# Kernel optimization log

Measured on AMD Instinct MI355X. Metric: run time of the kernel, lower is better.

## Reference

```python
import jax, jax.numpy as jnp
import numpy as np

B, S, E, H = 2, 2048, 512, 8
D = E // H
BETA = 0.5
SCALE = float(np.sqrt(D))


def setup_inputs() -> dict:
    key = jax.random.key(0)
    ks = jax.random.split(key, 22)
    inp = {}
    for i, n in enumerate(["qx", "qy", "kx", "ky", "vx", "vy"]):
        inp[n] = jax.random.normal(ks[i], (B, S, E), jnp.float32)
    wnames = ["Wqx", "Wqy", "Wkx", "Wky", "Wvx", "Wvy", "Wox", "Woy"]
    for i, n in enumerate(wnames):
        inp[n] = jax.random.normal(ks[6 + i], (E, E), jnp.float32) * 0.02
        inp["b" + n[1:]] = jnp.zeros((E,), jnp.float32)
    return inp


def _split_heads(x):
    # [B, S, E] -> [B, H, S, D]
    return x.reshape(B, S, H, D).transpose(0, 2, 1, 3)


def _merge_heads(x):
    # [B, H, S, D] -> [B, S, E]
    return x.transpose(0, 2, 1, 3).reshape(B, S, E)


def reference(qx, qy, kx, ky, vx, vy,
              Wqx, bqx, Wqy, bqy, Wkx, bkx, Wky, bky,
              Wvx, bvx, Wvy, bvy, Wox, box, Woy, boy):
    lin = lambda x, W, b: x @ W.T + b  # torch nn.Linear convention
    qxh = _split_heads(lin(qx, Wqx, bqx))
    qyh = _split_heads(lin(qy, Wqy, bqy))
    kxh = _split_heads(lin(kx, Wkx, bkx))
    kyh = _split_heads(lin(ky, Wky, bky))
    vxh = _split_heads(lin(vx, Wvx, bvx))
    vyh = _split_heads(lin(vy, Wvy, bvy))

    # polar decomposition of the bichannel: radius, angle
    aq = jnp.arctan2(qyh, qxh)  # [B,H,S,D]
    ak = jnp.arctan2(kyh, kxh)
    # mean_d cos(aq - ak) == (cos_q @ cos_k^T + sin_q @ sin_k^T) / D
    # (avoids the [B,H,Sq,Sk,D] angle_diff tensor; same math)
    phase = (jnp.einsum('bhqd,bhkd->bhqk', jnp.cos(aq), jnp.cos(ak))
             + jnp.einsum('bhqd,bhkd->bhqk', jnp.sin(aq), jnp.sin(ak))) / D

    rq = jnp.sqrt(qxh * qxh + qyh * qyh)
    rk = jnp.sqrt(kxh * kxh + kyh * kyh)
    mag = jnp.einsum('bhqd,bhkd->bhqk', rq, rk) / SCALE

    scores = BETA * phase + (1.0 - BETA) * mag  # [B,H,Sq,Sk]
    attn = jax.nn.softmax(scores, axis=-1)      # dropout is identity in eval

    ax = _merge_heads(jnp.einsum('bhqk,bhkd->bhqd', attn, vxh))
    ay = _merge_heads(jnp.einsum('bhqk,bhkd->bhqd', attn, vyh))
    return lin(ax, Wox, box), lin(ay, Woy, boy)
```

## Files before the change

kernel.cpp:

```cpp
#include <hip/hip_runtime.h>
#include <hip/hip_bf16.h>


#define N_ROWS 4096
#define EDIM 512
#define SEQ 2048
#define NHEAD 8
#define HDIM 64
#define CDIM 192
#define DV 128

#define PHASE_A 0.08838834764831845f
#define MAG_B   0.25f
#define SM_SHIFT 8.0f

typedef _Float16 half8 __attribute__((ext_vector_type(8)));
typedef float f32x4 __attribute__((ext_vector_type(4)));

__device__ inline void gload16(const void* g, void* l) {
    __builtin_amdgcn_global_load_lds(
        (const __attribute__((address_space(1))) unsigned int*)g,
        (__attribute__((address_space(3))) unsigned int*)l, 16, 0, 0);
}

#define KSW(r) (((((r) & 3) | (((r) >> 1) & 4))) << 4)

struct Cvt8 { const float* s[8]; _Float16* d[8]; };

__global__ __launch_bounds__(256) void cvt_fp16(Cvt8 j, int n8) {
    const float* s = j.s[blockIdx.y];
    _Float16* d = j.d[blockIdx.y];
    union U { _Float16 h[8]; uint4 u; };
    for (int i = blockIdx.x * 256 + threadIdx.x; i < n8; i += gridDim.x * 256) {
        const float4 f0 = ((const float4*)s)[2 * i];
        const float4 f1 = ((const float4*)s)[2 * i + 1];
        U u;
        u.h[0] = (_Float16)f0.x; u.h[1] = (_Float16)f0.y;
        u.h[2] = (_Float16)f0.z; u.h[3] = (_Float16)f0.w;
        u.h[4] = (_Float16)f1.x; u.h[5] = (_Float16)f1.y;
        u.h[6] = (_Float16)f1.z; u.h[7] = (_Float16)f1.w;
        ((uint4*)d)[i] = u.u;
    }
}

struct PairArgs {
    const void* x0;     const void* x1;
    const _Float16* w0; const _Float16* w1;
    const float* b0;    const float* b1;
    void* dst0;         void* dst1;
};

template <int FUSED>
__global__ __launch_bounds__(256, 3) void gemm16(PairArgs A0, PairArgs A1, PairArgs A2)
{
    __shared__ _Float16 smem[2][12288];

    const int tid = threadIdx.x;
    const int w = tid >> 6, l = tid & 63;
    const int g = l >> 4, ql = l & 15;
    const int wr = w >> 1, wc = w & 1;

    const int dd = blockIdx.x;
    const int xcd = dd & 7;
    const int sb = dd >> 3;
    int z_, mt, nb;
    if (FUSED) {
        const int zm = xcd * 12 + (sb >> 3);
        nb = sb & 7;
        z_ = zm >> 5;
        mt = zm & 31;
    } else {
        z_ = 0;
        mt = xcd * 4 + (sb >> 3);
        nb = sb & 7;
    }
    const PairArgs& A = FUSED ? (z_ == 0 ? A0 : (z_ == 1 ? A1 : A2)) : A0;
    const int z = z_;
    const int m0 = mt * 128;
    const int n0 = nb * 64;

    size_t srcA[2];
    #pragma unroll
    for (int i = 0; i < 2; ++i) {
        const int s = i * 256 + tid;
        const int row = s >> 2, c = s & 3;
        const int cs = c ^ ((row >> 1) & 3);
        srcA[i] = (size_t)(m0 + row) * EDIM + cs * 8;
    }
    const int rowB = tid >> 2;
    const int csB = (tid & 3) ^ ((rowB >> 1) & 3);
    const size_t srcB = (size_t)(n0 + rowB) * EDIM + csB * 8;

    const float* x0f = (const float*)A.x0;
    const float* x1f = (const float*)A.x1;
    const _Float16* x0h = (const _Float16*)A.x0;
    const _Float16* x1h = (const _Float16*)A.x1;

    float4 xr[2][2][2];

    #define LOADX(k0)                                                         \
        do { _Pragma("unroll")                                                \
          for (int i = 0; i < 2; ++i) {                                       \
              const float* p0 = x0f + srcA[i] + (k0);                         \
              const float* p1 = x1f + srcA[i] + (k0);                         \
              xr[0][i][0] = *(const float4*)p0;                               \
              xr[0][i][1] = *(const float4*)(p0 + 4);                         \
              xr[1][i][0] = *(const float4*)p1;                               \
              xr[1][i][1] = *(const float4*)(p1 + 4);                         \
          } } while (0)
    #define WRITEX(buf)                                                       \
        do { _Pragma("unroll")                                                \
          for (int arr = 0; arr < 2; ++arr) {                                 \
              _Pragma("unroll")                                               \
              for (int i = 0; i < 2; ++i) {                                   \
                  union { _Float16 h[8]; uint4 u; } t;                        \
                  _Pragma("unroll")                                           \
                  for (int jj = 0; jj < 4; ++jj) {                            \
                      t.h[jj]     = (_Float16)xr[arr][i][0][jj];              \
                      t.h[4 + jj] = (_Float16)xr[arr][i][1][jj];              \
                  }                                                           \
                  *(uint4*)&smem[buf][arr * 4096 + (i * 256 + tid) * 8] = t.u;\
              } } } while (0)
    #define STAGEX_LDS(buf, k0)                                               \
        do { _Pragma("unroll")                                                \
          for (int i = 0; i < 2; ++i) {                                       \
              gload16(x0h + srcA[i] + (k0),                                   \
                      &smem[buf][(i * 256 + w * 64) * 8]);                    \
              gload16(x1h + srcA[i] + (k0),                                   \
                      &smem[buf][4096 + (i * 256 + w * 64) * 8]);             \
          } } while (0)
    #define STAGEW(buf, k0)                                                   \
        do { gload16(A.w0 + srcB + (k0), &smem[buf][8192 + w * 512]);         \
             gload16(A.w1 + srcB + (k0), &smem[buf][10240 + w * 512]); } while (0)

    f32x4 acc0[4][2], acc1[4][2];
    #pragma unroll
    for (int f = 0; f < 4; ++f)
        #pragma unroll
        for (int e = 0; e < 2; ++e) {
            acc0[f][e] = (f32x4){0.f, 0.f, 0.f, 0.f};
            acc1[f][e] = (f32x4){0.f, 0.f, 0.f, 0.f};
        }

    auto COMPUTE = [&](int buf) {
        half8 af0[4], af1[4], bf0[2], bf1[2];
        #pragma unroll
        for (int f = 0; f < 4; ++f) {
            const int arow = wr * 64 + f * 16 + ql;
            const int ho = arow * 32 + (g ^ ((arow >> 1) & 3)) * 8;
            af0[f] = *(const half8*)&smem[buf][ho];
            af1[f] = *(const half8*)&smem[buf][4096 + ho];
        }
        #pragma unroll
        for (int e = 0; e < 2; ++e) {
            const int brow = wc * 32 + e * 16 + ql;
            const int ho = brow * 32 + (g ^ ((brow >> 1) & 3)) * 8;
            bf0[e] = *(const half8*)&smem[buf][8192 + ho];
            bf1[e] = *(const half8*)&smem[buf][10240 + ho];
        }
        #pragma unroll
        for (int f = 0; f < 4; ++f)
            #pragma unroll
            for (int e = 0; e < 2; ++e) {
                acc0[f][e] = __builtin_amdgcn_mfma_f32_16x16x32_f16(
                    af0[f], bf0[e], acc0[f][e], 0, 0, 0);
                acc1[f][e] = __builtin_amdgcn_mfma_f32_16x16x32_f16(
                    af1[f], bf1[e], acc1[f][e], 0, 0, 0);
            }
    };

    if (FUSED) {
        LOADX(0);
        WRITEX(0);
    } else {
        STAGEX_LDS(0, 0);
    }
    STAGEW(0, 0);

    for (int k0 = 0; k0 < EDIM; k0 += 32) {
        const int cur = (k0 >> 5) & 1, nxt = cur ^ 1;
        __syncthreads();
        const bool more = (k0 + 32) < EDIM;
        if (more) {
            if (FUSED) {
                LOADX(k0 + 32);
            } else {
                STAGEX_LDS(nxt, k0 + 32);
            }
            STAGEW(nxt, k0 + 32);
        }
        COMPUTE(cur);
        if (more && FUSED) {
            WRITEX(nxt);
        }
    }
    #undef LOADX
    #undef WRITEX
    #undef STAGEX_LDS
    #undef STAGEW

    #pragma unroll
    for (int f = 0; f < 4; ++f) {
        const int mb = m0 + wr * 64 + f * 16 + g * 4;
        #pragma unroll
        for (int e = 0; e < 2; ++e) {
            const int n = n0 + wc * 32 + e * 16 + ql;
            const float bias0 = A.b0[n];
            const float bias1 = A.b1[n];
            if (!FUSED) {
                float* o0 = (float*)A.dst0;
                float* o1 = (float*)A.dst1;
                #pragma unroll
                for (int r = 0; r < 4; ++r) {
                    const int m = mb + r;
                    o0[(size_t)m * EDIM + n] = acc0[f][e][r] + bias0;
                    o1[(size_t)m * EDIM + n] = acc1[f][e][r] + bias1;
                }
            } else {
                const int b = mb >> 11, s = mb & (SEQ - 1);
                const int h = nb;
                const int d = n & (HDIM - 1);
                const int bh = b * NHEAD + h;
                _Float16* dst = (_Float16*)A.dst0;
                if (z != 2) {
                    const size_t base = ((size_t)bh * SEQ + s) * CDIM + d;
                    #pragma unroll
                    for (int r = 0; r < 4; ++r) {
                        const float v0 = acc0[f][e][r] + bias0;
                        const float v1 = acc1[f][e][r] + bias1;
                        const float r2 = v0 * v0 + v1 * v1;
                        const float rm = sqrtf(r2);
                        float c, sn;
                        if (r2 > 0.f) { c = v0 / rm; sn = v1 / rm; }
                        else          { c = 1.f;     sn = 0.f; }
                        dst[base + (size_t)r * CDIM]       = (_Float16)(c  * PHASE_A);
                        dst[base + (size_t)r * CDIM + 64]  = (_Float16)(sn * PHASE_A);
                        dst[base + (size_t)r * CDIM + 128] = (_Float16)(rm * MAG_B);
                    }
                } else {
                    union Pk { _Float16 h[4]; uint2 u; } p0, p1;
                    #pragma unroll
                    for (int r = 0; r < 4; ++r) {
                        p0.h[r] = (_Float16)(acc0[f][e][r] + bias0);
                        p1.h[r] = (_Float16)(acc1[f][e][r] + bias1);
                    }
                    *(uint2*)&dst[((size_t)bh * DV + d) * SEQ + s]      = p0.u;
                    *(uint2*)&dst[((size_t)bh * DV + 64 + d) * SEQ + s] = p1.u;
                }
            }
        }
    }
}

__global__ __launch_bounds__(512, 2) void attn_mfma(
    const _Float16* __restrict__ Qg, const _Float16* __restrict__ Kg,
    const _Float16* __restrict__ Vg,
    _Float16* __restrict__ ax, _Float16* __restrict__ ay)
{
    __shared__ char smem[81920];

    const int tid = threadIdx.x;
    const int w  = tid >> 6;
    const int l  = tid & 63;
    const int g  = l >> 4;
    const int ql = l & 15;

    const int d  = blockIdx.x;
    const int xcd = d & 7;
    const int j   = d >> 3;
    const int bh  = xcd + 8 * (j >> 4);
    const int q0  = (j & 15) * 128;
    const int b  = bh >> 3, h = bh & 7;
    const int qrow = q0 + w * 16 + ql;

    half8 qf[6];
    {
        const char* qp = (const char*)(Qg + ((size_t)bh * SEQ + qrow) * CDIM);
        #pragma unroll
        for (int c = 0; c < 6; ++c) {
            uint4 u = *(const uint4*)(qp + c * 64 + g * 16);
            qf[c] = __builtin_bit_cast(half8, u);
        }
    }

    f32x4 o[8];
    #pragma unroll
    for (int vt = 0; vt < 8; ++vt) o[vt] = (f32x4){0.f, 0.f, 0.f, 0.f};
    float l_i = 0.f;

    const char* kgb = (const char*)(Kg + (size_t)bh * SEQ * CDIM);
    const char* vgb = (const char*)(Vg + (size_t)bh * DV * SEQ);

    int koff[3], vofs[2];
    #pragma unroll
    for (int i = 0; i < 3; ++i) {
        const int beta = (w * 3 + i) * 1024 + l * 16;
        const int r = beta / 384;
        const int cb = (beta - r * 384) ^ KSW(r);
        koff[i] = r * 384 + cb;
    }
    #pragma unroll
    for (int i = 0; i < 2; ++i) {
        const int beta = (w * 2 + i) * 1024 + l * 16;
        const int r = beta >> 7;
        const int cb = (beta & 127) ^ ((r & 7) << 4);
        vofs[i] = r * 4096 + cb;
    }

    const int rq = ((ql >> 2) << 3) + (ql & 3);
    const int kxor = ((ql & 3) | (((ql >> 2) & 1) << 2)) << 4;

    #define STAGE(kbase, vbase, kt0)                                          \
        do { _Pragma("unroll")                                                \
          for (int i = 0; i < 3; ++i)                                         \
              gload16(kgb + (size_t)(kt0) * 384 + koff[i],                    \
                      smem + (kbase) + (w * 3 + i) * 1024);                   \
          _Pragma("unroll")                                                   \
          for (int i = 0; i < 2; ++i)                                         \
              gload16(vgb + (size_t)(kt0) * 2 + vofs[i],                      \
                      smem + (vbase) + (w * 2 + i) * 1024); } while (0)

    auto COMPUTE = [&](const int kbase, const int vbase) {
        f32x4 st[4];
        __builtin_amdgcn_s_setprio(1);
        #pragma unroll
        for (int kt = 0; kt < 4; ++kt) {
            f32x4 acc = {0.f, 0.f, 0.f, 0.f};
            const int r_p = rq + (kt & 1) * 32 + ((kt >> 1) << 2);
            #pragma unroll
            for (int c = 0; c < 6; ++c) {
                uint4 u = *(const uint4*)(
                    smem + kbase + ((r_p * 384 + c * 64 + g * 16) ^ kxor));
                acc = __builtin_amdgcn_mfma_f32_16x16x32_f16(
                    __builtin_bit_cast(half8, u), qf[c], acc, 0, 0, 0);
            }
            st[kt] = acc;
        }
        __builtin_amdgcn_s_setprio(0);

        float rs = 0.f;
        #pragma unroll
        for (int kt = 0; kt < 4; ++kt)
            #pragma unroll
            for (int r = 0; r < 4; ++r) {
                const float p = __expf(st[kt][r] - SM_SHIFT);
                st[kt][r] = p; rs += p;
            }
        rs += __shfl_xor(rs, 16);
        rs += __shfl_xor(rs, 32);
        l_i += rs;

        half8 pf[2];
        #pragma unroll
        for (int ks = 0; ks < 2; ++ks) {
            union { _Float16 h[8]; half8 v; } u;
            u.h[0] = (_Float16)st[ks][0];     u.h[1] = (_Float16)st[ks][1];
            u.h[2] = (_Float16)st[ks][2];     u.h[3] = (_Float16)st[ks][3];
            u.h[4] = (_Float16)st[ks + 2][0]; u.h[5] = (_Float16)st[ks + 2][1];
            u.h[6] = (_Float16)st[ks + 2][2]; u.h[7] = (_Float16)st[ks + 2][3];
            pf[ks] = u.v;
        }

        __builtin_amdgcn_s_setprio(1);
        #pragma unroll
        for (int vt = 0; vt < 8; ++vt) {
            const int v = vt * 16 + ql;
            uint4 u0 = *(const uint4*)(
                smem + vbase + ((v * 128 + g * 16) ^ ((v & 7) << 4)));
            uint4 u1 = *(const uint4*)(
                smem + vbase + ((v * 128 + 64 + g * 16) ^ ((v & 7) << 4)));
            o[vt] = __builtin_amdgcn_mfma_f32_16x16x32_f16(
                pf[0], __builtin_bit_cast(half8, u0), o[vt], 0, 0, 0);
            o[vt] = __builtin_amdgcn_mfma_f32_16x16x32_f16(
                pf[1], __builtin_bit_cast(half8, u1), o[vt], 0, 0, 0);
        }
        __builtin_amdgcn_s_setprio(0);
    };

    STAGE(0, 49152, 0);
    for (int t = 0; t < 32; t += 2) {
        __syncthreads();
        STAGE(24576, 65536, (t + 1) * 64);
        COMPUTE(0, 49152);
        __syncthreads();
        if (t + 2 < 32) STAGE(0, 49152, (t + 2) * 64);
        COMPUTE(24576, 65536);
    }
    #undef STAGE

    const float invl = 1.f / l_i;
    const float fi0 = __shfl(invl, g * 4 + 0);
    const float fi1 = __shfl(invl, g * 4 + 1);
    const float fi2 = __shfl(invl, g * 4 + 2);
    const float fi3 = __shfl(invl, g * 4 + 3);
    #pragma unroll
    for (int vt = 0; vt < 8; ++vt) {
        const int v = vt * 16 + ql;
        _Float16* basep = (vt < 4) ? ax : ay;
        const int vv = v & 63;
        const float fi[4] = {fi0, fi1, fi2, fi3};
        #pragma unroll
        for (int r = 0; r < 4; ++r) {
            const int q = q0 + w * 16 + g * 4 + r;
            basep[((size_t)(b * SEQ + q)) * EDIM + h * HDIM + vv] =
                (_Float16)(o[vt][r] * fi[r]);
        }
    }
}

extern "C" void kernel_launch(void* const* d_in, const int* in_sizes, int n_in,
                              void* d_out, int out_size, void* d_ws, size_t ws_size,
                              hipStream_t stream)
{
    const float* act[6];
    for (int i = 0; i < 6; ++i) act[i] = (const float*)d_in[i];
    const float* W[8]; const float* Bv[8];
    for (int i = 0; i < 8; ++i) {
        W[i]  = (const float*)d_in[6 + 2 * i];
        Bv[i] = (const float*)d_in[7 + 2 * i];
    }

    float* outx = (float*)d_out;
    float* outy = outx + 2097152;

    _Float16* ws = (_Float16*)d_ws;
    _Float16* w16[8];
    for (int i = 0; i < 8; ++i) w16[i] = ws + (size_t)i * 262144;
    _Float16* Qt16 = ws + 2097152;
    _Float16* Kt16 = Qt16 + 6291456;
    _Float16* Vt16 = Kt16 + 6291456;
    _Float16* ax16 = Vt16 + 4194304;
    _Float16* ay16 = ax16 + 2097152;

    Cvt8 jw{};
    for (int i = 0; i < 8; ++i) { jw.s[i] = W[i]; jw.d[i] = w16[i]; }
    hipLaunchKernelGGL(cvt_fp16, dim3(128, 8), dim3(256), 0, stream, jw, 32768);

    PairArgs qa{act[0], act[1], w16[0], w16[1], Bv[0], Bv[1], Qt16, nullptr};
    PairArgs ka{act[2], act[3], w16[2], w16[3], Bv[2], Bv[3], Kt16, nullptr};
    PairArgs va{act[4], act[5], w16[4], w16[5], Bv[4], Bv[5], Vt16, nullptr};
    hipLaunchKernelGGL((gemm16<1>), dim3(768), dim3(256), 0, stream, qa, ka, va);

    hipLaunchKernelGGL(attn_mfma, dim3(256), dim3(512), 0, stream,
                       Qt16, Kt16, Vt16, ax16, ay16);

    PairArgs oa{ax16, ay16, w16[6], w16[7], Bv[6], Bv[7], outx, outy};
    hipLaunchKernelGGL((gemm16<0>), dim3(256), dim3(256), 0, stream, oa, oa, oa);
}
```

Measured before the change: 116.9 us.

## Process two query sub-tiles per wave in attention to reuse K/V fragments

The attention kernel now runs 4 waves of 256 threads instead of 8, and each wave handles 32 query rows as two 16-row halves. Each K and V fragment read from LDS feeds two MFMAs, which halves LDS read traffic per FLOP. Each thread now issues twice as many global-to-LDS staging loads. The cost is doubled accumulator and score registers per wave, half the waves per block, and launch bounds that allow only one block per CU, so there is less latency hiding.

```diff
diff --git a/kernel.cpp b/kernel.cpp
--- a/kernel.cpp
+++ b/kernel.cpp
@@ -252,7 +252,7 @@
     }
 }
 
-__global__ __launch_bounds__(512, 2) void attn_mfma(
+__global__ __launch_bounds__(256, 1) void attn_mfma(
     const _Float16* __restrict__ Qg, const _Float16* __restrict__ Kg,
     const _Float16* __restrict__ Vg,
     _Float16* __restrict__ ax, _Float16* __restrict__ ay)
@@ -271,37 +271,41 @@
     const int bh  = xcd + 8 * (j >> 4);
     const int q0  = (j & 15) * 128;
     const int b  = bh >> 3, h = bh & 7;
-    const int qrow = q0 + w * 16 + ql;
-
-    half8 qf[6];
-    {
+
+    half8 qf[2][6];
+    #pragma unroll
+    for (int hh = 0; hh < 2; ++hh) {
+        const int qrow = q0 + w * 32 + hh * 16 + ql;
         const char* qp = (const char*)(Qg + ((size_t)bh * SEQ + qrow) * CDIM);
         #pragma unroll
         for (int c = 0; c < 6; ++c) {
             uint4 u = *(const uint4*)(qp + c * 64 + g * 16);
-            qf[c] = __builtin_bit_cast(half8, u);
-        }
-    }
-
-    f32x4 o[8];
-    #pragma unroll
-    for (int vt = 0; vt < 8; ++vt) o[vt] = (f32x4){0.f, 0.f, 0.f, 0.f};
-    float l_i = 0.f;
+            qf[hh][c] = __builtin_bit_cast(half8, u);
+        }
+    }
+
+    f32x4 o0[8], o1[8];
+    #pragma unroll
+    for (int vt = 0; vt < 8; ++vt) {
+        o0[vt] = (f32x4){0.f, 0.f, 0.f, 0.f};
+        o1[vt] = (f32x4){0.f, 0.f, 0.f, 0.f};
+    }
+    float l_i0 = 0.f, l_i1 = 0.f;
 
     const char* kgb = (const char*)(Kg + (size_t)bh * SEQ * CDIM);
     const char* vgb = (const char*)(Vg + (size_t)bh * DV * SEQ);
 
-    int koff[3], vofs[2];
-    #pragma unroll
-    for (int i = 0; i < 3; ++i) {
-        const int beta = (w * 3 + i) * 1024 + l * 16;
+    int koff[6], vofs[4];
+    #pragma unroll
+    for (int i = 0; i < 6; ++i) {
+        const int beta = i * 4096 + w * 1024 + l * 16;
         const int r = beta / 384;
         const int cb = (beta - r * 384) ^ KSW(r);
         koff[i] = r * 384 + cb;
     }
     #pragma unroll
-    for (int i = 0; i < 2; ++i) {
-        const int beta = (w * 2 + i) * 1024 + l * 16;
+    for (int i = 0; i < 4; ++i) {
+        const int beta = i * 4096 + w * 1024 + l * 16;
         const int r = beta >> 7;
         const int cb = (beta & 127) ^ ((r & 7) << 4);
         vofs[i] = r * 4096 + cb;
@@ -312,67 +316,75 @@
 
     #define STAGE(kbase, vbase, kt0)                                          \
         do { _Pragma("unroll")                                                \
-          for (int i = 0; i < 3; ++i)                                         \
+          for (int i = 0; i < 6; ++i)                                         \
               gload16(kgb + (size_t)(kt0) * 384 + koff[i],                    \
-                      smem + (kbase) + (w * 3 + i) * 1024);                   \
+                      smem + (kbase) + i * 4096 + w * 1024);                  \
           _Pragma("unroll")                                                   \
-          for (int i = 0; i < 2; ++i)                                         \
+          for (int i = 0; i < 4; ++i)                                         \
               gload16(vgb + (size_t)(kt0) * 2 + vofs[i],                      \
-                      smem + (vbase) + (w * 2 + i) * 1024); } while (0)
+                      smem + (vbase) + i * 4096 + w * 1024); } while (0)
 
     auto COMPUTE = [&](const int kbase, const int vbase) {
-        f32x4 st[4];
+        f32x4 st0[4], st1[4];
         __builtin_amdgcn_s_setprio(1);
         #pragma unroll
         for (int kt = 0; kt < 4; ++kt) {
-            f32x4 acc = {0.f, 0.f, 0.f, 0.f};
+            f32x4 a0 = {0.f, 0.f, 0.f, 0.f};
+            f32x4 a1 = {0.f, 0.f, 0.f, 0.f};
             const int r_p = rq + (kt & 1) * 32 + ((kt >> 1) << 2);
             #pragma unroll
             for (int c = 0; c < 6; ++c) {
                 uint4 u = *(const uint4*)(
                     smem + kbase + ((r_p * 384 + c * 64 + g * 16) ^ kxor));
-                acc = __builtin_amdgcn_mfma_f32_16x16x32_f16(
-                    __builtin_bit_cast(half8, u), qf[c], acc, 0, 0, 0);
-            }
-            st[kt] = acc;
+                const half8 kf = __builtin_bit_cast(half8, u);
+                a0 = __builtin_amdgcn_mfma_f32_16x16x32_f16(kf, qf[0][c], a0, 0, 0, 0);
+                a1 = __builtin_amdgcn_mfma_f32_16x16x32_f16(kf, qf[1][c], a1, 0, 0, 0);
+            }
+            st0[kt] = a0; st1[kt] = a1;
         }
         __builtin_amdgcn_s_setprio(0);
 
-        float rs = 0.f;
+        float rs0 = 0.f, rs1 = 0.f;
         #pragma unroll
         for (int kt = 0; kt < 4; ++kt)
             #pragma unroll
             for (int r = 0; r < 4; ++r) {
-                const float p = __expf(st[kt][r] - SM_SHIFT);
-                st[kt][r] = p; rs += p;
-            }
-        rs += __shfl_xor(rs, 16);
-        rs += __shfl_xor(rs, 32);
-        l_i += rs;
-
-        half8 pf[2];
+                const float p0 = __expf(st0[kt][r] - SM_SHIFT);
+                const float p1 = __expf(st1[kt][r] - SM_SHIFT);
+                st0[kt][r] = p0; rs0 += p0;
+                st1[kt][r] = p1; rs1 += p1;
+            }
+        rs0 += __shfl_xor(rs0, 16); rs0 += __shfl_xor(rs0, 32); l_i0 += rs0;
+        rs1 += __shfl_xor(rs1, 16); rs1 += __shfl_xor(rs1, 32); l_i1 += rs1;
+
+        half8 pf0[2], pf1[2];
         #pragma unroll
         for (int ks = 0; ks < 2; ++ks) {
-            union { _Float16 h[8]; half8 v; } u;
-            u.h[0] = (_Float16)st[ks][0];     u.h[1] = (_Float16)st[ks][1];
-            u.h[2] = (_Float16)st[ks][2];     u.h[3] = (_Float16)st[ks][3];
-            u.h[4] = (_Float16)st[ks + 2][0]; u.h[5] = (_Float16)st[ks + 2][1];
-            u.h[6] = (_Float16)st[ks + 2][2]; u.h[7] = (_Float16)st[ks + 2][3];
-            pf[ks] = u.v;
+            union { _Float16 h[8]; half8 v; } u0, u1;
+            #pragma unroll
+            for (int r = 0; r < 4; ++r) {
+                u0.h[r]     = (_Float16)st0[ks][r];
+                u0.h[4 + r] = (_Float16)st0[ks + 2][r];
+                u1.h[r]     = (_Float16)st1[ks][r];
+                u1.h[4 + r] = (_Float16)st1[ks + 2][r];
+            }
+            pf0[ks] = u0.v; pf1[ks] = u1.v;
         }
 
         __builtin_amdgcn_s_setprio(1);
         #pragma unroll
         for (int vt = 0; vt < 8; ++vt) {
             const int v = vt * 16 + ql;
-            uint4 u0 = *(const uint4*)(
+            uint4 r0 = *(const uint4*)(
                 smem + vbase + ((v * 128 + g * 16) ^ ((v & 7) << 4)));
-            uint4 u1 = *(const uint4*)(
+            uint4 r1 = *(const uint4*)(
                 smem + vbase + ((v * 128 + 64 + g * 16) ^ ((v & 7) << 4)));
-            o[vt] = __builtin_amdgcn_mfma_f32_16x16x32_f16(
-                pf[0], __builtin_bit_cast(half8, u0), o[vt], 0, 0, 0);
-            o[vt] = __builtin_amdgcn_mfma_f32_16x16x32_f16(
-                pf[1], __builtin_bit_cast(half8, u1), o[vt], 0, 0, 0);
+            const half8 v0 = __builtin_bit_cast(half8, r0);
+            const half8 v1 = __builtin_bit_cast(half8, r1);
+            o0[vt] = __builtin_amdgcn_mfma_f32_16x16x32_f16(pf0[0], v0, o0[vt], 0, 0, 0);
+            o0[vt] = __builtin_amdgcn_mfma_f32_16x16x32_f16(pf0[1], v1, o0[vt], 0, 0, 0);
+            o1[vt] = __builtin_amdgcn_mfma_f32_16x16x32_f16(pf1[0], v0, o1[vt], 0, 0, 0);
+            o1[vt] = __builtin_amdgcn_mfma_f32_16x16x32_f16(pf1[1], v1, o1[vt], 0, 0, 0);
         }
         __builtin_amdgcn_s_setprio(0);
     };
@@ -388,22 +400,27 @@
     }
     #undef STAGE
 
-    const float invl = 1.f / l_i;
-    const float fi0 = __shfl(invl, g * 4 + 0);
-    const float fi1 = __shfl(invl, g * 4 + 1);
-    const float fi2 = __shfl(invl, g * 4 + 2);
-    const float fi3 = __shfl(invl, g * 4 + 3);
+    const float invl0 = 1.f / l_i0;
+    const float invl1 = 1.f / l_i1;
+    float fi0[4], fi1[4];
+    #pragma unroll
+    for (int r = 0; r < 4; ++r) {
+        fi0[r] = __shfl(invl0, g * 4 + r);
+        fi1[r] = __shfl(invl1, g * 4 + r);
+    }
     #pragma unroll
     for (int vt = 0; vt < 8; ++vt) {
         const int v = vt * 16 + ql;
         _Float16* basep = (vt < 4) ? ax : ay;
         const int vv = v & 63;
-        const float fi[4] = {fi0, fi1, fi2, fi3};
         #pragma unroll
         for (int r = 0; r < 4; ++r) {
-            const int q = q0 + w * 16 + g * 4 + r;
-            basep[((size_t)(b * SEQ + q)) * EDIM + h * HDIM + vv] =
-                (_Float16)(o[vt][r] * fi[r]);
+            const int qA = q0 + w * 32 + g * 4 + r;
+            const int qB = qA + 16;
+            basep[((size_t)(b * SEQ + qA)) * EDIM + h * HDIM + vv] =
+                (_Float16)(o0[vt][r] * fi0[r]);
+            basep[((size_t)(b * SEQ + qB)) * EDIM + h * HDIM + vv] =
+                (_Float16)(o1[vt][r] * fi1[r]);
         }
     }
 }
@@ -441,7 +458,7 @@
     PairArgs va{act[4], act[5], w16[4], w16[5], Bv[4], Bv[5], Vt16, nullptr};
     hipLaunchKernelGGL((gemm16<1>), dim3(768), dim3(256), 0, stream, qa, ka, va);
 
-    hipLaunchKernelGGL(attn_mfma, dim3(256), dim3(512), 0, stream,
+    hipLaunchKernelGGL(attn_mfma, dim3(256), dim3(256), 0, stream,
                        Qt16, Kt16, Vt16, ax16, ay16);
 
     PairArgs oa{ax16, ay16, w16[6], w16[7], Bv[6], Bv[7], outx, outy};
```

Result: slower. 129.0 us (+10.3%).

## Split attention key tiles across wave pairs with two query sub-tiles per wave

Applied to the files above, without the earlier changes.

Each pair of waves now shares 32 query rows, and each wave holds two 16-row Q fragments but handles only half of every 64-key tile. Every K and V fragment read from LDS is reused for two MFMAs, which halves the LDS read traffic per MFMA. At the end, partial output accumulators and row sums are combined across the wave pair through shared memory. In exchange, register use doubles for the O and Q fragments, and the reduction adds an extra barrier and epilogue work.

```diff
diff --git a/kernel.cpp b/kernel.cpp
--- a/kernel.cpp
+++ b/kernel.cpp
@@ -264,6 +264,8 @@
     const int l  = tid & 63;
     const int g  = l >> 4;
     const int ql = l & 15;
+    const int tg = w >> 1;
+    const int kh = w & 1;
 
     const int d  = blockIdx.x;
     const int xcd = d & 7;
@@ -271,22 +273,25 @@
     const int bh  = xcd + 8 * (j >> 4);
     const int q0  = (j & 15) * 128;
     const int b  = bh >> 3, h = bh & 7;
-    const int qrow = q0 + w * 16 + ql;
-
-    half8 qf[6];
-    {
+
+    half8 qf[2][6];
+    #pragma unroll
+    for (int hh = 0; hh < 2; ++hh) {
+        const int qrow = q0 + tg * 32 + hh * 16 + ql;
         const char* qp = (const char*)(Qg + ((size_t)bh * SEQ + qrow) * CDIM);
         #pragma unroll
         for (int c = 0; c < 6; ++c) {
             uint4 u = *(const uint4*)(qp + c * 64 + g * 16);
-            qf[c] = __builtin_bit_cast(half8, u);
-        }
-    }
-
-    f32x4 o[8];
-    #pragma unroll
-    for (int vt = 0; vt < 8; ++vt) o[vt] = (f32x4){0.f, 0.f, 0.f, 0.f};
-    float l_i = 0.f;
+            qf[hh][c] = __builtin_bit_cast(half8, u);
+        }
+    }
+
+    f32x4 o[2][8];
+    #pragma unroll
+    for (int hh = 0; hh < 2; ++hh)
+        #pragma unroll
+        for (int vt = 0; vt < 8; ++vt) o[hh][vt] = (f32x4){0.f, 0.f, 0.f, 0.f};
+    float l_i[2] = {0.f, 0.f};
 
     const char* kgb = (const char*)(Kg + (size_t)bh * SEQ * CDIM);
     const char* vgb = (const char*)(Vg + (size_t)bh * DV * SEQ);
@@ -321,58 +326,61 @@
                       smem + (vbase) + (w * 2 + i) * 1024); } while (0)
 
     auto COMPUTE = [&](const int kbase, const int vbase) {
-        f32x4 st[4];
+        f32x4 st[2][2];
         __builtin_amdgcn_s_setprio(1);
         #pragma unroll
-        for (int kt = 0; kt < 4; ++kt) {
-            f32x4 acc = {0.f, 0.f, 0.f, 0.f};
-            const int r_p = rq + (kt & 1) * 32 + ((kt >> 1) << 2);
+        for (int kt2 = 0; kt2 < 2; ++kt2) {
+            f32x4 a0 = {0.f, 0.f, 0.f, 0.f};
+            f32x4 a1 = {0.f, 0.f, 0.f, 0.f};
+            const int r_p = rq + kh * 32 + (kt2 << 2);
             #pragma unroll
             for (int c = 0; c < 6; ++c) {
                 uint4 u = *(const uint4*)(
                     smem + kbase + ((r_p * 384 + c * 64 + g * 16) ^ kxor));
-                acc = __builtin_amdgcn_mfma_f32_16x16x32_f16(
-                    __builtin_bit_cast(half8, u), qf[c], acc, 0, 0, 0);
-            }
-            st[kt] = acc;
+                const half8 kf = __builtin_bit_cast(half8, u);
+                a0 = __builtin_amdgcn_mfma_f32_16x16x32_f16(kf, qf[0][c], a0, 0, 0, 0);
+                a1 = __builtin_amdgcn_mfma_f32_16x16x32_f16(kf, qf[1][c], a1, 0, 0, 0);
+            }
+            st[0][kt2] = a0; st[1][kt2] = a1;
         }
         __builtin_amdgcn_s_setprio(0);
 
-        float rs = 0.f;
-        #pragma unroll
-        for (int kt = 0; kt < 4; ++kt)
+        #pragma unroll
+        for (int hh = 0; hh < 2; ++hh) {
+            float rs = 0.f;
+            #pragma unroll
+            for (int kt2 = 0; kt2 < 2; ++kt2)
+                #pragma unroll
+                for (int r = 0; r < 4; ++r) {
+                    const float p = __expf(st[hh][kt2][r] - SM_SHIFT);
+                    st[hh][kt2][r] = p; rs += p;
+                }
+            rs += __shfl_xor(rs, 16);
+            rs += __shfl_xor(rs, 32);
+            l_i[hh] += rs;
+        }
+
+        half8 pf[2];
+        #pragma unroll
+        for (int hh = 0; hh < 2; ++hh) {
+            union { _Float16 hhv[8]; half8 v; } u;
             #pragma unroll
             for (int r = 0; r < 4; ++r) {
-                const float p = __expf(st[kt][r] - SM_SHIFT);
-                st[kt][r] = p; rs += p;
-            }
-        rs += __shfl_xor(rs, 16);
-        rs += __shfl_xor(rs, 32);
-        l_i += rs;
-
-        half8 pf[2];
-        #pragma unroll
-        for (int ks = 0; ks < 2; ++ks) {
-            union { _Float16 h[8]; half8 v; } u;
-            u.h[0] = (_Float16)st[ks][0];     u.h[1] = (_Float16)st[ks][1];
-            u.h[2] = (_Float16)st[ks][2];     u.h[3] = (_Float16)st[ks][3];
-            u.h[4] = (_Float16)st[ks + 2][0]; u.h[5] = (_Float16)st[ks + 2][1];
-            u.h[6] = (_Float16)st[ks + 2][2]; u.h[7] = (_Float16)st[ks + 2][3];
-            pf[ks] = u.v;
+                u.hhv[r]     = (_Float16)st[hh][0][r];
+                u.hhv[4 + r] = (_Float16)st[hh][1][r];
+            }
+            pf[hh] = u.v;
         }
 
         __builtin_amdgcn_s_setprio(1);
         #pragma unroll
         for (int vt = 0; vt < 8; ++vt) {
             const int v = vt * 16 + ql;
-            uint4 u0 = *(const uint4*)(
-                smem + vbase + ((v * 128 + g * 16) ^ ((v & 7) << 4)));
-            uint4 u1 = *(const uint4*)(
-                smem + vbase + ((v * 128 + 64 + g * 16) ^ ((v & 7) << 4)));
-            o[vt] = __builtin_amdgcn_mfma_f32_16x16x32_f16(
-                pf[0], __builtin_bit_cast(half8, u0), o[vt], 0, 0, 0);
-            o[vt] = __builtin_amdgcn_mfma_f32_16x16x32_f16(
-                pf[1], __builtin_bit_cast(half8, u1), o[vt], 0, 0, 0);
+            uint4 u = *(const uint4*)(
+                smem + vbase + ((v * 128 + kh * 64 + g * 16) ^ ((v & 7) << 4)));
+            const half8 vf = __builtin_bit_cast(half8, u);
+            o[0][vt] = __builtin_amdgcn_mfma_f32_16x16x32_f16(pf[0], vf, o[0][vt], 0, 0, 0);
+            o[1][vt] = __builtin_amdgcn_mfma_f32_16x16x32_f16(pf[1], vf, o[1][vt], 0, 0, 0);
         }
         __builtin_amdgcn_s_setprio(0);
     };
@@ -388,22 +396,44 @@
     }
     #undef STAGE
 
-    const float invl = 1.f / l_i;
-    const float fi0 = __shfl(invl, g * 4 + 0);
-    const float fi1 = __shfl(invl, g * 4 + 1);
-    const float fi2 = __shfl(invl, g * 4 + 2);
-    const float fi3 = __shfl(invl, g * 4 + 3);
-    #pragma unroll
-    for (int vt = 0; vt < 8; ++vt) {
-        const int v = vt * 16 + ql;
-        _Float16* basep = (vt < 4) ? ax : ay;
-        const int vv = v & 63;
-        const float fi[4] = {fi0, fi1, fi2, fi3};
+    __syncthreads();
+    if (kh == 1) {
+        char* base = smem + tg * 16384;
+        #pragma unroll
+        for (int hh = 0; hh < 2; ++hh)
+            #pragma unroll
+            for (int vt = 0; vt < 8; ++vt)
+                *(f32x4*)(base + hh * 8192 + vt * 1024 + l * 16) = o[hh][vt];
+        *(float2*)(smem + 65536 + tg * 512 + l * 8) =
+            make_float2(l_i[0], l_i[1]);
+    }
+    __syncthreads();
+    if (kh == 0) {
+        const char* base = smem + tg * 16384;
+        const float2 lp = *(const float2*)(smem + 65536 + tg * 512 + l * 8);
+        const float inv0 = 1.f / (l_i[0] + lp.x);
+        const float inv1 = 1.f / (l_i[1] + lp.y);
+        float fi[2][4];
         #pragma unroll
         for (int r = 0; r < 4; ++r) {
-            const int q = q0 + w * 16 + g * 4 + r;
-            basep[((size_t)(b * SEQ + q)) * EDIM + h * HDIM + vv] =
-                (_Float16)(o[vt][r] * fi[r]);
+            fi[0][r] = __shfl(inv0, g * 4 + r);
+            fi[1][r] = __shfl(inv1, g * 4 + r);
+        }
+        #pragma unroll
+        for (int hh = 0; hh < 2; ++hh) {
+            #pragma unroll
+            for (int vt = 0; vt < 8; ++vt) {
+                const f32x4 op = *(const f32x4*)(base + hh * 8192 + vt * 1024 + l * 16);
+                const int v = vt * 16 + ql;
+                _Float16* basep = (vt < 4) ? ax : ay;
+                const int vv = v & 63;
+                #pragma unroll
+                for (int r = 0; r < 4; ++r) {
+                    const int q = q0 + tg * 32 + hh * 16 + g * 4 + r;
+                    basep[((size_t)(b * SEQ + q)) * EDIM + h * HDIM + vv] =
+                        (_Float16)((o[hh][vt][r] + op[r]) * fi[hh][r]);
+                }
+            }
         }
     }
 }
```

Result: no change. 116.8 us (-0.1%).

## Split key tiles across warp pairs in attention and reduce partial outputs via LDS

Applied to the files above, without the earlier changes.

Each attention block now covers 64 query rows instead of 128, and the grid doubles to 512 blocks. Within a block, pairs of warps share the same 16 query rows, and each warp handles half of every 64-key tile. At the end the partial O accumulators and row sums are combined through shared memory. This doubles the number of blocks to fill the GPU better, at the cost of loading K/V twice per query and adding a final cross-warp reduction.

```diff
diff --git a/kernel.cpp b/kernel.cpp
--- a/kernel.cpp
+++ b/kernel.cpp
@@ -264,17 +264,19 @@
     const int l  = tid & 63;
     const int g  = l >> 4;
     const int ql = l & 15;
+    const int tg = w >> 1;
+    const int kh = w & 1;
 
     const int d  = blockIdx.x;
     const int xcd = d & 7;
     const int j   = d >> 3;
-    const int bh  = xcd + 8 * (j >> 4);
-    const int q0  = (j & 15) * 128;
+    const int bh  = xcd + 8 * (j >> 5);
+    const int q0  = (j & 31) * 64;
     const int b  = bh >> 3, h = bh & 7;
-    const int qrow = q0 + w * 16 + ql;
 
     half8 qf[6];
     {
+        const int qrow = q0 + tg * 16 + ql;
         const char* qp = (const char*)(Qg + ((size_t)bh * SEQ + qrow) * CDIM);
         #pragma unroll
         for (int c = 0; c < 6; ++c) {
@@ -321,58 +323,54 @@
                       smem + (vbase) + (w * 2 + i) * 1024); } while (0)
 
     auto COMPUTE = [&](const int kbase, const int vbase) {
-        f32x4 st[4];
+        f32x4 st[2];
         __builtin_amdgcn_s_setprio(1);
         #pragma unroll
-        for (int kt = 0; kt < 4; ++kt) {
-            f32x4 acc = {0.f, 0.f, 0.f, 0.f};
-            const int r_p = rq + (kt & 1) * 32 + ((kt >> 1) << 2);
+        for (int kt2 = 0; kt2 < 2; ++kt2) {
+            f32x4 a0 = {0.f, 0.f, 0.f, 0.f};
+            const int r_p = rq + kh * 32 + (kt2 << 2);
             #pragma unroll
             for (int c = 0; c < 6; ++c) {
                 uint4 u = *(const uint4*)(
                     smem + kbase + ((r_p * 384 + c * 64 + g * 16) ^ kxor));
-                acc = __builtin_amdgcn_mfma_f32_16x16x32_f16(
-                    __builtin_bit_cast(half8, u), qf[c], acc, 0, 0, 0);
-            }
-            st[kt] = acc;
+                a0 = __builtin_amdgcn_mfma_f32_16x16x32_f16(
+                    __builtin_bit_cast(half8, u), qf[c], a0, 0, 0, 0);
+            }
+            st[kt2] = a0;
         }
         __builtin_amdgcn_s_setprio(0);
 
         float rs = 0.f;
         #pragma unroll
-        for (int kt = 0; kt < 4; ++kt)
+        for (int kt2 = 0; kt2 < 2; ++kt2)
             #pragma unroll
             for (int r = 0; r < 4; ++r) {
-                const float p = __expf(st[kt][r] - SM_SHIFT);
-                st[kt][r] = p; rs += p;
+                const float p = __expf(st[kt2][r] - SM_SHIFT);
+                st[kt2][r] = p; rs += p;
             }
         rs += __shfl_xor(rs, 16);
         rs += __shfl_xor(rs, 32);
         l_i += rs;
 
-        half8 pf[2];
-        #pragma unroll
-        for (int ks = 0; ks < 2; ++ks) {
-            union { _Float16 h[8]; half8 v; } u;
-            u.h[0] = (_Float16)st[ks][0];     u.h[1] = (_Float16)st[ks][1];
-            u.h[2] = (_Float16)st[ks][2];     u.h[3] = (_Float16)st[ks][3];
-            u.h[4] = (_Float16)st[ks + 2][0]; u.h[5] = (_Float16)st[ks + 2][1];
-            u.h[6] = (_Float16)st[ks + 2][2]; u.h[7] = (_Float16)st[ks + 2][3];
-            pf[ks] = u.v;
+        half8 pf;
+        {
+            union { _Float16 hv[8]; half8 v; } u;
+            #pragma unroll
+            for (int r = 0; r < 4; ++r) {
+                u.hv[r]     = (_Float16)st[0][r];
+                u.hv[4 + r] = (_Float16)st[1][r];
+            }
+            pf = u.v;
         }
 
         __builtin_amdgcn_s_setprio(1);
         #pragma unroll
         for (int vt = 0; vt < 8; ++vt) {
             const int v = vt * 16 + ql;
-            uint4 u0 = *(const uint4*)(
-                smem + vbase + ((v * 128 + g * 16) ^ ((v & 7) << 4)));
-            uint4 u1 = *(const uint4*)(
-                smem + vbase + ((v * 128 + 64 + g * 16) ^ ((v & 7) << 4)));
+            uint4 u = *(const uint4*)(
+                smem + vbase + ((v * 128 + kh * 64 + g * 16) ^ ((v & 7) << 4)));
             o[vt] = __builtin_amdgcn_mfma_f32_16x16x32_f16(
-                pf[0], __builtin_bit_cast(half8, u0), o[vt], 0, 0, 0);
-            o[vt] = __builtin_amdgcn_mfma_f32_16x16x32_f16(
-                pf[1], __builtin_bit_cast(half8, u1), o[vt], 0, 0, 0);
+                pf, __builtin_bit_cast(half8, u), o[vt], 0, 0, 0);
         }
         __builtin_amdgcn_s_setprio(0);
     };
@@ -388,22 +386,34 @@
     }
     #undef STAGE
 
-    const float invl = 1.f / l_i;
-    const float fi0 = __shfl(invl, g * 4 + 0);
-    const float fi1 = __shfl(invl, g * 4 + 1);
-    const float fi2 = __shfl(invl, g * 4 + 2);
-    const float fi3 = __shfl(invl, g * 4 + 3);
-    #pragma unroll
-    for (int vt = 0; vt < 8; ++vt) {
-        const int v = vt * 16 + ql;
-        _Float16* basep = (vt < 4) ? ax : ay;
-        const int vv = v & 63;
-        const float fi[4] = {fi0, fi1, fi2, fi3};
-        #pragma unroll
-        for (int r = 0; r < 4; ++r) {
-            const int q = q0 + w * 16 + g * 4 + r;
-            basep[((size_t)(b * SEQ + q)) * EDIM + h * HDIM + vv] =
-                (_Float16)(o[vt][r] * fi[r]);
+    __syncthreads();
+    if (kh == 1) {
+        char* base = smem + tg * 8192;
+        #pragma unroll
+        for (int vt = 0; vt < 8; ++vt)
+            *(f32x4*)(base + vt * 1024 + l * 16) = o[vt];
+        *(float*)(smem + 32768 + tg * 256 + l * 4) = l_i;
+    }
+    __syncthreads();
+    if (kh == 0) {
+        const char* base = smem + tg * 8192;
+        const float lp = *(const float*)(smem + 32768 + tg * 256 + l * 4);
+        const float inv = 1.f / (l_i + lp);
+        float fi[4];
+        #pragma unroll
+        for (int r = 0; r < 4; ++r) fi[r] = __shfl(inv, g * 4 + r);
+        #pragma unroll
+        for (int vt = 0; vt < 8; ++vt) {
+            const f32x4 op = *(const f32x4*)(base + vt * 1024 + l * 16);
+            const int v = vt * 16 + ql;
+            _Float16* basep = (vt < 4) ? ax : ay;
+            const int vv = v & 63;
+            #pragma unroll
+            for (int r = 0; r < 4; ++r) {
+                const int q = q0 + tg * 16 + g * 4 + r;
+                basep[((size_t)(b * SEQ + q)) * EDIM + h * HDIM + vv] =
+                    (_Float16)((o[vt][r] + op[r]) * fi[r]);
+            }
         }
     }
 }
@@ -441,7 +451,7 @@
     PairArgs va{act[4], act[5], w16[4], w16[5], Bv[4], Bv[5], Vt16, nullptr};
     hipLaunchKernelGGL((gemm16<1>), dim3(768), dim3(256), 0, stream, qa, ka, va);
 
-    hipLaunchKernelGGL(attn_mfma, dim3(256), dim3(512), 0, stream,
+    hipLaunchKernelGGL(attn_mfma, dim3(512), dim3(512), 0, stream,
                        Qt16, Kt16, Vt16, ax16, ay16);
 
     PairArgs oa{ax16, ay16, w16[6], w16[7], Bv[6], Bv[7], outx, outy};
```

Result: slower. 139.5 us (+19.3%).
